# Performance work log

Hardware: AMD Instinct MI355X
Metric: run time of the kernel (lower is better)

Reference implementation:

```python
import jax, jax.numpy as jnp
import numpy as np

DIM = 768
HEAD_DIM = 64          # num_head arg (per-head dim)
N_HEADS = DIM // HEAD_DIM  # 12
B, N = 4, 2048


def setup_inputs() -> dict:
    key = jax.random.key(0)
    ks = jax.random.split(key, 7)
    s = DIM ** -0.5
    return {
        "x":  jax.random.normal(ks[0], (B, N, DIM), jnp.float32),
        "wq": jax.random.normal(ks[1], (DIM, DIM), jnp.float32) * s,
        "bq": jax.random.normal(ks[2], (DIM,), jnp.float32) * 0.01,
        "wk": jax.random.normal(ks[3], (DIM, DIM), jnp.float32) * s,
        "bk": jax.random.normal(ks[4], (DIM,), jnp.float32) * 0.01,
        "wv": jax.random.normal(ks[5], (DIM, DIM), jnp.float32) * s,
        "bv": jax.random.normal(ks[6], (DIM,), jnp.float32) * 0.01,
    }


def reference(x, wq, bq, wk, bk, wv, bv):
    # torch Linear: y = x @ W.T + b
    q = x @ wq.T + bq
    k = x @ wk.T + bk
    v = x @ wv.T + bv
    # split heads: b n (h d) -> b h n d
    def split(t):
        return t.reshape(B, N, N_HEADS, HEAD_DIM).transpose(0, 2, 1, 3)
    q, k, v = split(q), split(k), split(v)
    scale = HEAD_DIM ** -0.5
    logit = jnp.einsum("bhnd,bhmd->bhnm", q, k) * scale  # [B,H,N,N]
    attn = jax.nn.softmax(logit, axis=-1)
    out = jnp.einsum("bhnm,bhmd->bhnd", attn, v)
    # concat heads: b h n d -> b n (h d)
    return out.transpose(0, 2, 1, 3).reshape(B, N, DIM)
```

## Files before the change

kernel.cpp:

```cpp
#include <hip/hip_runtime.h>
#include <cstdint>

#define NSEQ 2048
#define DIM  768
#define NH   12
#define HD   64

typedef __attribute__((ext_vector_type(8)))  short bf16x8;
typedef __attribute__((ext_vector_type(4)))  float f32x4;
typedef __attribute__((ext_vector_type(16))) float f32x16;
typedef __attribute__((ext_vector_type(4)))  int   i32x4;
typedef unsigned short u16;

#define MFMA16(a,b,c) __builtin_amdgcn_mfma_f32_16x16x32_bf16(a,b,c,0,0,0)
#define MFMA32(a,b,c) __builtin_amdgcn_mfma_f32_32x32x16_bf16(a,b,c,0,0,0)

#define QSCALE 0.1803368801111204f

__device__ __forceinline__ u16 f2bf(float f){
  unsigned u = __builtin_bit_cast(unsigned, f);
  return (u16)((u + 0x7fffu + ((u >> 16) & 1u)) >> 16);
}
__device__ __forceinline__ int cvtpk(float a, float b){
  int r;
  asm("v_cvt_pk_bf16_f32 %0, %1, %2" : "=v"(r) : "v"(a), "v"(b));
  return r;
}

typedef __attribute__((address_space(1))) void gvoid_t;
typedef __attribute__((address_space(3))) void lvoid_t;
__device__ __forceinline__ void g2l16(const void* g, void* l){
  __builtin_amdgcn_global_load_lds((gvoid_t*)g, (lvoid_t*)l, 16, 0, 0);
}

__global__ __launch_bounds__(256) void convert_all(
    const float* __restrict__ x,  const float* __restrict__ wq,
    const float* __restrict__ wk, const float* __restrict__ wv,
    u16* __restrict__ xb, u16* __restrict__ wb){
  int blk = blockIdx.x, tid = threadIdx.x;
  const float* src; u16* dst; long idx;
  if (blk < 6144){ src = x; dst = xb; idx = (long)blk*256 + tid; }
  else {
    int r = blk - 6144; int s = r / 576; r -= s*576;
    src = (s==0) ? wq : (s==1) ? wk : wv;
    dst = wb + (long)s * (768*768);
    idx = (long)r*256 + tid;
  }
  float4 v = ((const float4*)src)[idx];
  ushort4 o;
  o.x = f2bf(v.x); o.y = f2bf(v.y); o.z = f2bf(v.z); o.w = f2bf(v.w);
  ((ushort4*)dst)[idx] = o;
}

__global__ __launch_bounds__(256,3) void qkv_gemm(
    const u16* __restrict__ xb, const u16* __restrict__ wb,
    const float* __restrict__ bq, const float* __restrict__ bk,
    const float* __restrict__ bv,
    u16* __restrict__ Qo, u16* __restrict__ Ko, u16* __restrict__ Vo){
  __shared__ __align__(16) u16 ldsX[128*64];
  __shared__ __align__(16) u16 ldsW[96*64];
  int tid  = threadIdx.x;
  int w    = tid >> 6, lane = tid & 63;
  int xcd  = blockIdx.x & 7, j = blockIdx.x >> 3;
  int bm   = xcd*8 + j/24, bn = j%24;
  int wm   = w >> 1, wn = w & 1;
  int l15  = lane & 15, g = lane >> 4;
  int srow = lane >> 3;
  int scol = ((lane & 7) ^ srow) * 8;

  const u16* xg = xb + (long)bm*128*768;
  const u16* wg = wb + (long)bn*96*768;

  f32x4 acc[4][3] = {};

  for (int k0 = 0; k0 < 768; k0 += 64){
    if (k0) __syncthreads();
    #pragma unroll
    for (int jj = 0; jj < 4; jj++){
      int rr = (w*4 + jj)*8 + srow;
      g2l16(xg + (long)rr*768 + k0 + scol, &ldsX[(w*4 + jj)*512]);
    }
    #pragma unroll
    for (int jj = 0; jj < 3; jj++){
      int rr = (w*3 + jj)*8 + srow;
      g2l16(wg + (long)rr*768 + k0 + scol, &ldsW[(w*3 + jj)*512]);
    }
    __syncthreads();
    #pragma unroll
    for (int ks = 0; ks < 2; ks++){
      bf16x8 af[4], bfr[3];
      #pragma unroll
      for (int im = 0; im < 4; im++){
        int row = wm*64 + im*16 + l15;
        af[im] = *(const bf16x8*)&ldsX[row*64 + (((ks*4 + g) ^ (row & 7))*8)];
      }
      #pragma unroll
      for (int in = 0; in < 3; in++){
        int row = wn*48 + in*16 + l15;
        bfr[in] = *(const bf16x8*)&ldsW[row*64 + (((ks*4 + g) ^ (row & 7))*8)];
      }
      #pragma unroll
      for (int im = 0; im < 4; im++)
        #pragma unroll
        for (int in = 0; in < 3; in++)
          acc[im][in] = MFMA16(af[im], bfr[in], acc[im][in]);
    }
  }

  int seg = bn >> 3;
  const float* bias = (seg==0) ? bq : (seg==1) ? bk : bv;
  #pragma unroll
  for (int in = 0; in < 3; in++){
    int o  = bn*96 + wn*48 + in*16 + l15;
    int oo = o - seg*768;
    int h  = oo >> 6, d = oo & 63;
    float bb = bias[oo];
    #pragma unroll
    for (int im = 0; im < 4; im++){
      int t  = bm*128 + wm*64 + im*16 + g*4;
      int bi = t >> 11, n0 = t & 2047;
      f32x4 a = acc[im][in];
      if (seg == 2){
        ushort4 pk;
        pk.x = f2bf(a[0] + bb); pk.y = f2bf(a[1] + bb);
        pk.z = f2bf(a[2] + bb); pk.w = f2bf(a[3] + bb);
        *(ushort4*)&Vo[((long)(bi*NH + h)*HD + d)*NSEQ + n0] = pk;
      } else if (seg == 0){
        #pragma unroll
        for (int r = 0; r < 4; r++)
          Qo[((long)(bi*NH + h)*NSEQ + n0 + r)*HD + d] = f2bf((a[r] + bb)*QSCALE);
      } else {
        #pragma unroll
        for (int r = 0; r < 4; r++)
          Ko[((long)(bi*NH + h)*NSEQ + n0 + r)*HD + d] = f2bf(a[r] + bb);
      }
    }
  }
}

__global__ __launch_bounds__(256,3) void attn(
    const u16* __restrict__ Q, const u16* __restrict__ K,
    const u16* __restrict__ VT, float* __restrict__ out){
  __shared__ __align__(16) u16 kls[2][64*64];
  __shared__ __align__(16) u16 vls[2][64*64];
  int tid = threadIdx.x;
  int w   = tid >> 6, lane = tid & 63;
  int xcd = blockIdx.x & 7, j = blockIdx.x >> 3;
  int bh  = xcd*6 + (j >> 4), qc = j & 15;
  int b   = bh / NH, h = bh - b*NH;
  int l31 = lane & 31, hi = lane >> 5;
  int srow = lane >> 3;
  int scol = ((lane & 7) ^ srow) * 8;

  const u16* Qb = Q  + (long)bh*NSEQ*HD;
  const u16* Kb = K  + (long)bh*NSEQ*HD;
  const u16* Vb = VT + (long)bh*HD*NSEQ;

  int r0 = qc*128 + w*32;
  bf16x8 qf[4];
  {
    const u16* qrow = Qb + (long)(r0 + l31)*HD;
    #pragma unroll
    for (int dk = 0; dk < 4; dk++)
      qf[dk] = *(const bf16x8*)&qrow[dk*16 + hi*8];
  }

  f32x16 oa[2] = {};
  float ls = 0.f;

#define STAGE(c0, bf)                                                         \
  {                                                                           \
    _Pragma("unroll")                                                         \
    for (int jj = 0; jj < 2; jj++){                                           \
      int rr = jj*32 + w*8;                                                   \
      g2l16(Kb + (long)((c0) + rr + srow)*HD + scol,  &kls[bf][rr*64]);       \
      g2l16(Vb + (long)(rr + srow)*NSEQ + (c0) + scol, &vls[bf][rr*64]);      \
    }                                                                         \
  }

#define KH(bf, kh)                                                            \
  {                                                                           \
    bf16x8 kf[4];                                                             \
    _Pragma("unroll")                                                         \
    for (int dk = 0; dk < 4; dk++)                                            \
      kf[dk] = *(const bf16x8*)                                               \
        &kls[bf][((kh)*32 + l31)*64 + (((dk*2 + hi) ^ (l31 & 7))*8)];         \
    f32x16 T = {};                                                            \
    __builtin_amdgcn_s_setprio(1);                                            \
    _Pragma("unroll")                                                         \
    for (int dk = 0; dk < 4; dk++)                                            \
      T = MFMA32(kf[dk], qf[dk], T);                                          \
    __builtin_amdgcn_s_setprio(0);                                            \
    int PD[4][2];                                                             \
    _Pragma("unroll")                                                         \
    for (int q = 0; q < 4; q++){                                              \
      float p0 = __builtin_amdgcn_exp2f(T[q*4+0]);                            \
      float p1 = __builtin_amdgcn_exp2f(T[q*4+1]);                            \
      float p2 = __builtin_amdgcn_exp2f(T[q*4+2]);                            \
      float p3 = __builtin_amdgcn_exp2f(T[q*4+3]);                            \
      ls += (p0 + p1) + (p2 + p3);                                            \
      PD[q][0] = cvtpk(p0, p1);                                               \
      PD[q][1] = cvtpk(p2, p3);                                               \
    }                                                                         \
    _Pragma("unroll")                                                         \
    for (int kc = 0; kc < 2; kc++){                                           \
      int a0 = PD[2*kc][0], b0 = PD[2*kc+1][0];                               \
      int a1 = PD[2*kc][1], b1 = PD[2*kc+1][1];                               \
      asm("v_permlane32_swap_b32 %0, %1" : "+v"(a0), "+v"(b0));               \
      asm("v_permlane32_swap_b32 %0, %1" : "+v"(a1), "+v"(b1));               \
      i32x4 pr;                                                               \
      pr[0] = a0; pr[1] = a1; pr[2] = b0; pr[3] = b1;                         \
      bf16x8 pf = __builtin_bit_cast(bf16x8, pr);                             \
      __builtin_amdgcn_s_setprio(1);                                          \
      _Pragma("unroll")                                                       \
      for (int dt = 0; dt < 2; dt++){                                         \
        bf16x8 vf = *(const bf16x8*)                                          \
          &vls[bf][(dt*32 + l31)*64 + ((((kh)*4 + kc*2 + hi) ^ (l31 & 7))*8)];\
        oa[dt] = MFMA32(vf, pf, oa[dt]);                                      \
      }                                                                       \
      __builtin_amdgcn_s_setprio(0);                                          \
    }                                                                         \
  }

  STAGE(0, 0);
  __syncthreads();
  for (int i = 0; i < 32; i++){
    int cb = i & 1, nb = cb ^ 1;
    STAGE(((i+1) & 31)*64, nb);
    __builtin_amdgcn_sched_barrier(0);
    asm volatile("s_waitcnt vmcnt(4) lgkmcnt(0)" ::: "memory");
    __builtin_amdgcn_sched_barrier(0);
    __builtin_amdgcn_s_barrier();
    KH(cb, 0);
    KH(cb, 1);
    __builtin_amdgcn_sched_barrier(0);
    asm volatile("s_waitcnt lgkmcnt(0)" ::: "memory");
    __builtin_amdgcn_sched_barrier(0);
    __builtin_amdgcn_s_barrier();
  }
#undef STAGE
#undef KH

  ls += __shfl_xor(ls, 32);
  float inv = 1.f / ls;

  float* op = &out[(long)(b*NSEQ + r0 + l31)*DIM + h*HD];
  #pragma unroll
  for (int dt = 0; dt < 2; dt++)
    #pragma unroll
    for (int rq = 0; rq < 4; rq++){
      f32x4 v;
      v[0] = oa[dt][rq*4+0]; v[1] = oa[dt][rq*4+1];
      v[2] = oa[dt][rq*4+2]; v[3] = oa[dt][rq*4+3];
      v *= inv;
      *(f32x4*)&op[dt*32 + rq*8 + hi*4] = v;
    }
}

extern "C" void kernel_launch(void* const* d_in, const int* in_sizes, int n_in,
                              void* d_out, int out_size, void* d_ws, size_t ws_size,
                              hipStream_t stream){
  (void)in_sizes; (void)n_in; (void)out_size; (void)ws_size;
  const float* x  = (const float*)d_in[0];
  const float* wq = (const float*)d_in[1];
  const float* bq = (const float*)d_in[2];
  const float* wk = (const float*)d_in[3];
  const float* bk = (const float*)d_in[4];
  const float* wv = (const float*)d_in[5];
  const float* bv = (const float*)d_in[6];

  char* ws = (char*)d_ws;
  u16* xb = (u16*)ws;
  u16* wb = (u16*)(ws + 12582912);
  u16* Qp = (u16*)(ws + 16121856);
  u16* Kp = (u16*)(ws + 28704768);
  u16* Vp = (u16*)(ws + 41287680);

  convert_all<<<7872, 256, 0, stream>>>(x, wq, wk, wv, xb, wb);
  qkv_gemm<<<1536, 256, 0, stream>>>(xb, wb, bq, bk, bv, Qp, Kp, Vp);
  attn<<<768, 256, 0, stream>>>(Qp, Kp, Vp, (float*)d_out);
}
```

Measured before the change: 189.1 us.

## Enlarge QKV GEMM tile to 256x96 and use 32x32 MFMA

The QKV projection GEMM now computes a 256x96 output tile per block instead of 128x96. Each wave owns 64 rows across all 96 columns and uses 32x32x16 MFMA instructions in place of 16x16x32. This halves the grid, improves reuse of the weight tile per block, and cuts LDS fragment loads per MFMA. In exchange it uses more LDS, which may lower occupancy, and the grid of 768 blocks gives fewer waves to hide latency. The epilogue store pattern is adjusted for the 32x32 accumulator layout.

```diff
diff --git a/kernel.cpp b/kernel.cpp
--- a/kernel.cpp
+++ b/kernel.cpp
@@ -57,28 +57,27 @@
     const float* __restrict__ bq, const float* __restrict__ bk,
     const float* __restrict__ bv,
     u16* __restrict__ Qo, u16* __restrict__ Ko, u16* __restrict__ Vo){
-  __shared__ __align__(16) u16 ldsX[128*64];
+  __shared__ __align__(16) u16 ldsX[256*64];
   __shared__ __align__(16) u16 ldsW[96*64];
   int tid  = threadIdx.x;
   int w    = tid >> 6, lane = tid & 63;
   int xcd  = blockIdx.x & 7, j = blockIdx.x >> 3;
-  int bm   = xcd*8 + j/24, bn = j%24;
-  int wm   = w >> 1, wn = w & 1;
-  int l15  = lane & 15, g = lane >> 4;
+  int bm   = xcd*4 + j/24, bn = j%24;
+  int l31  = lane & 31, hi = lane >> 5;
   int srow = lane >> 3;
   int scol = ((lane & 7) ^ srow) * 8;
 
-  const u16* xg = xb + (long)bm*128*768;
+  const u16* xg = xb + (long)bm*256*768;
   const u16* wg = wb + (long)bn*96*768;
 
-  f32x4 acc[4][3] = {};
+  f32x16 acc[2][3] = {};
 
   for (int k0 = 0; k0 < 768; k0 += 64){
     if (k0) __syncthreads();
     #pragma unroll
-    for (int jj = 0; jj < 4; jj++){
-      int rr = (w*4 + jj)*8 + srow;
-      g2l16(xg + (long)rr*768 + k0 + scol, &ldsX[(w*4 + jj)*512]);
+    for (int jj = 0; jj < 8; jj++){
+      int rr = (w*8 + jj)*8 + srow;
+      g2l16(xg + (long)rr*768 + k0 + scol, &ldsX[(w*8 + jj)*512]);
     }
     #pragma unroll
     for (int jj = 0; jj < 3; jj++){
@@ -87,23 +86,23 @@
     }
     __syncthreads();
     #pragma unroll
-    for (int ks = 0; ks < 2; ks++){
-      bf16x8 af[4], bfr[3];
+    for (int ks = 0; ks < 4; ks++){
+      bf16x8 af[2], bfr[3];
       #pragma unroll
-      for (int im = 0; im < 4; im++){
-        int row = wm*64 + im*16 + l15;
-        af[im] = *(const bf16x8*)&ldsX[row*64 + (((ks*4 + g) ^ (row & 7))*8)];
+      for (int im = 0; im < 2; im++){
+        int row = w*64 + im*32 + l31;
+        af[im] = *(const bf16x8*)&ldsX[row*64 + (((ks*2 + hi) ^ (row & 7))*8)];
       }
       #pragma unroll
       for (int in = 0; in < 3; in++){
-        int row = wn*48 + in*16 + l15;
-        bfr[in] = *(const bf16x8*)&ldsW[row*64 + (((ks*4 + g) ^ (row & 7))*8)];
+        int row = in*32 + l31;
+        bfr[in] = *(const bf16x8*)&ldsW[row*64 + (((ks*2 + hi) ^ (row & 7))*8)];
       }
       #pragma unroll
-      for (int im = 0; im < 4; im++)
+      for (int im = 0; im < 2; im++)
         #pragma unroll
         for (int in = 0; in < 3; in++)
-          acc[im][in] = MFMA16(af[im], bfr[in], acc[im][in]);
+          acc[im][in] = MFMA32(af[im], bfr[in], acc[im][in]);
     }
   }
 
@@ -111,28 +110,36 @@
   const float* bias = (seg==0) ? bq : (seg==1) ? bk : bv;
   #pragma unroll
   for (int in = 0; in < 3; in++){
-    int o  = bn*96 + wn*48 + in*16 + l15;
+    int o  = bn*96 + in*32 + l31;
     int oo = o - seg*768;
     int h  = oo >> 6, d = oo & 63;
     float bb = bias[oo];
     #pragma unroll
-    for (int im = 0; im < 4; im++){
-      int t  = bm*128 + wm*64 + im*16 + g*4;
-      int bi = t >> 11, n0 = t & 2047;
-      f32x4 a = acc[im][in];
+    for (int im = 0; im < 2; im++){
+      int mb = bm*256 + w*64 + im*32;
+      int bi = mb >> 11, n0 = mb & 2047;
+      f32x16 a = acc[im][in];
       if (seg == 2){
-        ushort4 pk;
-        pk.x = f2bf(a[0] + bb); pk.y = f2bf(a[1] + bb);
-        pk.z = f2bf(a[2] + bb); pk.w = f2bf(a[3] + bb);
-        *(ushort4*)&Vo[((long)(bi*NH + h)*HD + d)*NSEQ + n0] = pk;
+        u16* vp = &Vo[((long)(bi*NH + h)*HD + d)*NSEQ + n0];
+        #pragma unroll
+        for (int q4 = 0; q4 < 4; q4++){
+          ushort4 pk;
+          pk.x = f2bf(a[q4*4+0] + bb); pk.y = f2bf(a[q4*4+1] + bb);
+          pk.z = f2bf(a[q4*4+2] + bb); pk.w = f2bf(a[q4*4+3] + bb);
+          *(ushort4*)&vp[q4*8 + hi*4] = pk;
+        }
       } else if (seg == 0){
         #pragma unroll
-        for (int r = 0; r < 4; r++)
-          Qo[((long)(bi*NH + h)*NSEQ + n0 + r)*HD + d] = f2bf((a[r] + bb)*QSCALE);
+        for (int rq = 0; rq < 16; rq++){
+          int m = n0 + (rq&3) + 8*(rq>>2) + 4*hi;
+          Qo[((long)(bi*NH + h)*NSEQ + m)*HD + d] = f2bf((a[rq] + bb)*QSCALE);
+        }
       } else {
         #pragma unroll
-        for (int r = 0; r < 4; r++)
-          Ko[((long)(bi*NH + h)*NSEQ + n0 + r)*HD + d] = f2bf(a[r] + bb);
+        for (int rq = 0; rq < 16; rq++){
+          int m = n0 + (rq&3) + 8*(rq>>2) + 4*hi;
+          Ko[((long)(bi*NH + h)*NSEQ + m)*HD + d] = f2bf(a[rq] + bb);
+        }
       }
     }
   }
@@ -277,6 +284,6 @@
   u16* Vp = (u16*)(ws + 41287680);
 
   convert_all<<<7872, 256, 0, stream>>>(x, wq, wk, wv, xb, wb);
-  qkv_gemm<<<1536, 256, 0, stream>>>(xb, wb, bq, bk, bv, Qp, Kp, Vp);
+  qkv_gemm<<<768, 256, 0, stream>>>(xb, wb, bq, bk, bv, Qp, Kp, Vp);
   attn<<<768, 256, 0, stream>>>(Qp, Kp, Vp, (float*)d_out);
 }
```

Result: no change. 190.6 us (+0.8%).
